# Optimization experiments

Measured on AMD Instinct MI355X. Metric: run time of the kernel, lower is better.

The kernel has to match this reference:

```python
import jax, jax.numpy as jnp
import numpy as np

B, OBS, H, A, E = 131072, 194, 64, 5, 3  # batch, obs dim, hidden, max_action_dim, n event types


def setup_inputs() -> dict:
    key = jax.random.key(0)
    ks = jax.random.split(key, 16)
    s = lambda k, shape, std=0.1: (jax.random.normal(k, shape, dtype=jnp.float32) * std)
    return {
        "x": jax.random.normal(ks[0], (B, OBS), dtype=jnp.float32),
        "action": jax.random.randint(ks[1], (B,), 0, A),
        "W1": s(ks[2], (OBS, H)), "b1": jnp.zeros((H,), jnp.float32),
        "W2": s(ks[3], (H, H)),   "b2": jnp.zeros((H,), jnp.float32),
        "Wh": s(ks[4], (E, H, A), 0.01), "bh": jnp.zeros((E, A), jnp.float32),
        "Wc1": s(ks[5], (OBS, H)), "bc1": jnp.zeros((H,), jnp.float32),
        "Wc2": s(ks[6], (H, H)),   "bc2": jnp.zeros((H,), jnp.float32),
        "Wc3": s(ks[7], (H, 1)),   "bc3": jnp.zeros((1,), jnp.float32),
    }


def reference(x, action, W1, b1, W2, b2, Wh, bh, Wc1, bc1, Wc2, bc2, Wc3, bc3):
    # shared trunk
    feat = jnp.tanh(jnp.tanh(x @ W1 + b1) @ W2 + b2)          # [B, H]
    # route each sample to one of E heads via argmax of first 3 obs dims
    ev = jnp.argmax(x[:, :E], axis=1)                          # [B] int
    all_logits = jnp.einsum('bh,eha->bea', feat, Wh) + bh      # [B, E, A]
    logits = jnp.take_along_axis(
        all_logits, jnp.broadcast_to(ev[:, None, None], (x.shape[0], 1, A)), axis=1
    )[:, 0]                                                    # [B, A]
    logp_all = jax.nn.log_softmax(logits, axis=-1)             # [B, A]
    logp = jnp.take_along_axis(logp_all, action[:, None], axis=1)[:, 0]  # [B]
    entropy = -jnp.sum(jnp.exp(logp_all) * logp_all, axis=-1)  # [B]
    # critic
    value = jnp.tanh(jnp.tanh(x @ Wc1 + bc1) @ Wc2 + bc2) @ Wc3 + bc3    # [B, 1]
    return action, logp, entropy, value
```

## Files before the change

### kernel.cpp

```cpp
#include <hip/hip_runtime.h>
#include <hip/hip_bf16.h>

constexpr int Bt  = 131072;
constexpr int OBS = 194;
constexpr int Hd  = 64;
constexpr int NT  = 256;
constexpr int MT  = 64;
constexpr int HS  = 72;
constexpr int LS  = 18;

constexpr int W1B_OFF  = 0;
constexpr int WC1B_OFF = 28672;
constexpr int W2B_OFF  = 57344;
constexpr int WC2B_OFF = 65536;
constexpr int WHB_OFF  = 73728;

typedef short bf8   __attribute__((ext_vector_type(8)));
typedef float f32x4 __attribute__((ext_vector_type(4)));

__device__ __forceinline__ short f2bs(float f) {
    union { __hip_bfloat16 h; short s; } u;
    u.h = __float2bfloat16(f);
    return u.s;
}
__device__ __forceinline__ float bs2f(short s) {
    union { short s; __hip_bfloat16 h; } u;
    u.s = s;
    return __bfloat162float(u.h);
}
__device__ __forceinline__ float fast_tanh(float v) {
    v = fminf(fmaxf(v, -15.f), 15.f);
    float e = __expf(2.f * v);
    return (e - 1.f) * __builtin_amdgcn_rcpf(e + 1.f);
}

__global__ void __launch_bounds__(256) prep(
    const float* __restrict__ W1, const float* __restrict__ W2,
    const float* __restrict__ Wh, const float* __restrict__ Wc1,
    const float* __restrict__ Wc2, const float* __restrict__ Wc3,
    short* __restrict__ ws)
{
    const int gid = blockIdx.x * 256 + threadIdx.x;
    const int gsz = gridDim.x * 256;

    for (int i = gid; i < 28672; i += gsz) {
        int j = i & 7, l = (i >> 3) & 63, nt = (i >> 9) & 3, kb = i >> 11;
        int k = kb * 32 + ((l >> 4) << 3) + j;
        int n = nt * 16 + (l & 15);
        short v1 = 0, v2 = 0;
        if (k < OBS) {
            v1 = f2bs(W1[k * 64 + n]);
            v2 = f2bs(Wc1[k * 64 + n]);
        }
        ws[W1B_OFF + i]  = v1;
        ws[WC1B_OFF + i] = v2;
    }
    for (int i = gid; i < 8192; i += gsz) {
        int j = i & 7, l = (i >> 3) & 63, nt = (i >> 9) & 3, kb = i >> 11;
        int k = kb * 32 + ((l >> 4) << 3) + j;
        int n = nt * 16 + (l & 15);
        ws[W2B_OFF + i]  = f2bs(W2[k * 64 + n]);
        ws[WC2B_OFF + i] = f2bs(Wc2[k * 64 + n]);
    }
    for (int i = gid; i < 1024; i += gsz) {
        int j = i & 7, l = (i >> 3) & 63, kb = i >> 9;
        int k = kb * 32 + ((l >> 4) << 3) + j;
        int cc = l & 15;
        float v;
        if (cc == 15) v = Wc3[k];
        else { int e = cc / 5, a = cc - 5 * e; v = Wh[(e * 64 + k) * 5 + a]; }
        ws[WHB_OFF + i] = f2bs(v);
    }
}

__global__ void __launch_bounds__(NT, 4) fused_ac(
    const float* __restrict__ x, const int* __restrict__ act_in,
    const float* __restrict__ b1, const float* __restrict__ b2,
    const float* __restrict__ bh, const float* __restrict__ bc1,
    const float* __restrict__ bc2, const float* __restrict__ bc3,
    const short* __restrict__ ws,
    float* __restrict__ out)
{
    __shared__ __align__(16) short hA[4][16 * HS];
    __shared__ __align__(16) short hC[4][16 * HS];
    __shared__ short logitb[4][16 * LS];
    __shared__ float valb[4][16];

    const int t  = threadIdx.x;
    const int w  = t >> 6;
    const int l  = t & 63;
    const int q  = l >> 4;
    const int c  = l & 15;
    const int b0 = blockIdx.x * MT;

    const bf8* __restrict__ fW1  = reinterpret_cast<const bf8*>(ws + W1B_OFF);
    const bf8* __restrict__ fWc1 = reinterpret_cast<const bf8*>(ws + WC1B_OFF);
    const bf8* __restrict__ fW2  = reinterpret_cast<const bf8*>(ws + W2B_OFF);
    const bf8* __restrict__ fWc2 = reinterpret_cast<const bf8*>(ws + WC2B_OFF);
    const bf8* __restrict__ fWh  = reinterpret_cast<const bf8*>(ws + WHB_OFF);

    short* ha = hA[w];
    short* hc = hC[w];

    f32x4 aa[4], ac[4];
    #pragma unroll
    for (int nt = 0; nt < 4; ++nt) {
        aa[nt] = f32x4{0.f, 0.f, 0.f, 0.f};
        ac[nt] = f32x4{0.f, 0.f, 0.f, 0.f};
    }
    {
        const float* xr = x + (size_t)(b0 + w * 16 + c) * OBS;
        #pragma unroll
        for (int kb = 0; kb < 6; ++kb) {
            const float2* p = reinterpret_cast<const float2*>(xr + kb * 32 + q * 8);
            float2 v0 = p[0], v1 = p[1], v2 = p[2], v3 = p[3];
            bf8 a;
            a[0] = f2bs(v0.x); a[1] = f2bs(v0.y); a[2] = f2bs(v1.x); a[3] = f2bs(v1.y);
            a[4] = f2bs(v2.x); a[5] = f2bs(v2.y); a[6] = f2bs(v3.x); a[7] = f2bs(v3.y);
            #pragma unroll
            for (int nt = 0; nt < 4; ++nt) {
                aa[nt] = __builtin_amdgcn_mfma_f32_16x16x32_bf16(a, fW1 [(kb * 4 + nt) * 64 + l], aa[nt], 0, 0, 0);
                ac[nt] = __builtin_amdgcn_mfma_f32_16x16x32_bf16(a, fWc1[(kb * 4 + nt) * 64 + l], ac[nt], 0, 0, 0);
            }
        }
        bf8 a6 = {0, 0, 0, 0, 0, 0, 0, 0};
        if (q == 0) {
            float2 v = *reinterpret_cast<const float2*>(xr + 192);
            a6[0] = f2bs(v.x); a6[1] = f2bs(v.y);
        }
        #pragma unroll
        for (int nt = 0; nt < 4; ++nt) {
            aa[nt] = __builtin_amdgcn_mfma_f32_16x16x32_bf16(a6, fW1 [(6 * 4 + nt) * 64 + l], aa[nt], 0, 0, 0);
            ac[nt] = __builtin_amdgcn_mfma_f32_16x16x32_bf16(a6, fWc1[(6 * 4 + nt) * 64 + l], ac[nt], 0, 0, 0);
        }
    }
    #pragma unroll
    for (int nt = 0; nt < 4; ++nt) {
        float ba = b1[nt * 16 + c], bc = bc1[nt * 16 + c];
        #pragma unroll
        for (int r = 0; r < 4; ++r) {
            ha[(q * 4 + r) * HS + nt * 16 + c] = f2bs(fast_tanh(aa[nt][r] + ba));
            hc[(q * 4 + r) * HS + nt * 16 + c] = f2bs(fast_tanh(ac[nt][r] + bc));
        }
    }

    #pragma unroll
    for (int nt = 0; nt < 4; ++nt) {
        aa[nt] = f32x4{0.f, 0.f, 0.f, 0.f};
        ac[nt] = f32x4{0.f, 0.f, 0.f, 0.f};
    }
    #pragma unroll
    for (int kb = 0; kb < 2; ++kb) {
        bf8 xa = *reinterpret_cast<const bf8*>(&ha[c * HS + kb * 32 + q * 8]);
        bf8 xc = *reinterpret_cast<const bf8*>(&hc[c * HS + kb * 32 + q * 8]);
        #pragma unroll
        for (int nt = 0; nt < 4; ++nt) {
            aa[nt] = __builtin_amdgcn_mfma_f32_16x16x32_bf16(xa, fW2 [(kb * 4 + nt) * 64 + l], aa[nt], 0, 0, 0);
            ac[nt] = __builtin_amdgcn_mfma_f32_16x16x32_bf16(xc, fWc2[(kb * 4 + nt) * 64 + l], ac[nt], 0, 0, 0);
        }
    }
    #pragma unroll
    for (int nt = 0; nt < 4; ++nt) {
        float ba = b2[nt * 16 + c], bc = bc2[nt * 16 + c];
        #pragma unroll
        for (int r = 0; r < 4; ++r) {
            ha[(q * 4 + r) * HS + nt * 16 + c] = f2bs(fast_tanh(aa[nt][r] + ba));
            hc[(q * 4 + r) * HS + nt * 16 + c] = f2bs(fast_tanh(ac[nt][r] + bc));
        }
    }

    {
        f32x4 lg = f32x4{0.f, 0.f, 0.f, 0.f};
        f32x4 vv = f32x4{0.f, 0.f, 0.f, 0.f};
        #pragma unroll
        for (int kb = 0; kb < 2; ++kb) {
            bf8 bw = fWh[kb * 64 + l];
            bf8 fa = *reinterpret_cast<const bf8*>(&ha[c * HS + kb * 32 + q * 8]);
            bf8 fc = *reinterpret_cast<const bf8*>(&hc[c * HS + kb * 32 + q * 8]);
            lg = __builtin_amdgcn_mfma_f32_16x16x32_bf16(fa, bw, lg, 0, 0, 0);
            vv = __builtin_amdgcn_mfma_f32_16x16x32_bf16(fc, bw, vv, 0, 0, 0);
        }
        short* lw = logitb[w];
        #pragma unroll
        for (int r = 0; r < 4; ++r)
            lw[(q * 4 + r) * LS + c] = f2bs(lg[r]);
        if (c == 15) {
            float bc3v = bc3[0];
            #pragma unroll
            for (int r = 0; r < 4; ++r)
                valb[w][q * 4 + r] = vv[r] + bc3v;
        }
    }

    {
        int m  = c;
        int gm = b0 + w * 16 + m;
        const float* xr = x + (size_t)gm * OBS;
        float x0 = xr[0], x1 = xr[1], x2 = xr[2];
        int ev = 0; float best = x0;
        if (x1 > best) { best = x1; ev = 1; }
        if (x2 > best) { ev = 2; }
        const short* lw = logitb[w];
        float lg[5];
        #pragma unroll
        for (int a = 0; a < 5; ++a)
            lg[a] = bs2f(lw[m * LS + ev * 5 + a]) + bh[ev * 5 + a];
        float mx = lg[0];
        #pragma unroll
        for (int a = 1; a < 5; ++a) mx = fmaxf(mx, lg[a]);
        float se = 0.f;
        #pragma unroll
        for (int a = 0; a < 5; ++a) se += __expf(lg[a] - mx);
        float lse = __logf(se) + mx;
        int act = act_in[gm];
        float lsel = lg[0];
        #pragma unroll
        for (int a = 1; a < 5; ++a) lsel = (act == a) ? lg[a] : lsel;
        float ent = 0.f;
        #pragma unroll
        for (int a = 0; a < 5; ++a) { float lp = lg[a] - lse; ent -= __expf(lp) * lp; }

        if (l < 16) {
            out[gm]          = (float)act;
            out[Bt + gm]     = lsel - lse;
            out[2 * Bt + gm] = ent;
            out[3 * Bt + gm] = valb[w][m];
        }
    }
}

extern "C" void kernel_launch(void* const* d_in, const int* in_sizes, int n_in,
                              void* d_out, int out_size, void* d_ws, size_t ws_size,
                              hipStream_t stream) {
    const float* x   = (const float*)d_in[0];
    const int*   act = (const int*)  d_in[1];
    const float* W1  = (const float*)d_in[2];
    const float* b1  = (const float*)d_in[3];
    const float* W2  = (const float*)d_in[4];
    const float* b2  = (const float*)d_in[5];
    const float* Wh  = (const float*)d_in[6];
    const float* bh  = (const float*)d_in[7];
    const float* Wc1 = (const float*)d_in[8];
    const float* bc1 = (const float*)d_in[9];
    const float* Wc2 = (const float*)d_in[10];
    const float* bc2 = (const float*)d_in[11];
    const float* Wc3 = (const float*)d_in[12];
    const float* bc3 = (const float*)d_in[13];
    float* out = (float*)d_out;
    short* ws  = (short*)d_ws;

    hipLaunchKernelGGL(prep, dim3(64), dim3(256), 0, stream,
                       W1, W2, Wh, Wc1, Wc2, Wc3, ws);
    hipLaunchKernelGGL(fused_ac, dim3(Bt / MT), dim3(NT), 0, stream,
                       x, act, b1, b2, bh, bc1, bc2, bc3, ws, out);
}
```

Before: 201.9 us.

## Fold biases into MFMA, permute hidden layout for packed stores, shrink blocks

Folds the layer-1 bias into the padded K slot of the weight matrix, with a constant 1 appended to the input. Initializes the layer-2 and head accumulators with their biases. Permutes the hidden-unit order in the W2 and head weight packing so each lane can write four consecutive bf16 activations with one packed 64-bit LDS store, using paired bf16 conversion. Computes the argmax event from the x values already loaded, dropping the second global read of x, and reduces blocks to 128 threads with a higher occupancy hint. These changes cut scalar LDS stores, conversions, bias adds and redundant global loads, but rounding the bias to bf16 adds small precision error.

```diff
diff --git a/kernel.cpp b/kernel.cpp
--- a/kernel.cpp
+++ b/kernel.cpp
@@ -3,10 +3,9 @@
 
 constexpr int Bt  = 131072;
 constexpr int OBS = 194;
-constexpr int Hd  = 64;
-constexpr int NT  = 256;
-constexpr int MT  = 64;
-constexpr int HS  = 72;
+constexpr int NT  = 128;
+constexpr int MT  = 32;
+constexpr int RS  = 72;
 constexpr int LS  = 18;
 
 constexpr int W1B_OFF  = 0;
@@ -17,6 +16,7 @@
 
 typedef short bf8   __attribute__((ext_vector_type(8)));
 typedef float f32x4 __attribute__((ext_vector_type(4)));
+typedef unsigned int u32;
 
 __device__ __forceinline__ short f2bs(float f) {
     union { __hip_bfloat16 h; short s; } u;
@@ -28,6 +28,11 @@
     u.s = s;
     return __bfloat162float(u.h);
 }
+__device__ __forceinline__ u32 pk2(float a, float b) {
+    union { __hip_bfloat162 h; u32 u; } r;
+    r.h = __float22bfloat162_rn(float2{a, b});
+    return r.u;
+}
 __device__ __forceinline__ float fast_tanh(float v) {
     v = fminf(fmaxf(v, -15.f), 15.f);
     float e = __expf(2.f * v);
@@ -35,8 +40,9 @@
 }
 
 __global__ void __launch_bounds__(256) prep(
-    const float* __restrict__ W1, const float* __restrict__ W2,
-    const float* __restrict__ Wh, const float* __restrict__ Wc1,
+    const float* __restrict__ W1, const float* __restrict__ b1,
+    const float* __restrict__ W2, const float* __restrict__ Wh,
+    const float* __restrict__ Wc1, const float* __restrict__ bc1,
     const float* __restrict__ Wc2, const float* __restrict__ Wc3,
     short* __restrict__ ws)
 {
@@ -51,47 +57,51 @@
         if (k < OBS) {
             v1 = f2bs(W1[k * 64 + n]);
             v2 = f2bs(Wc1[k * 64 + n]);
+        } else if (k == OBS) {
+            v1 = f2bs(b1[n]);
+            v2 = f2bs(bc1[n]);
         }
         ws[W1B_OFF + i]  = v1;
         ws[WC1B_OFF + i] = v2;
     }
     for (int i = gid; i < 8192; i += gsz) {
         int j = i & 7, l = (i >> 3) & 63, nt = (i >> 9) & 3, kb = i >> 11;
-        int k = kb * 32 + ((l >> 4) << 3) + j;
+        int s = kb * 32 + ((l >> 4) << 3) + j;
+        int kp = (s & 3) * 16 + (s >> 2);
         int n = nt * 16 + (l & 15);
-        ws[W2B_OFF + i]  = f2bs(W2[k * 64 + n]);
-        ws[WC2B_OFF + i] = f2bs(Wc2[k * 64 + n]);
+        ws[W2B_OFF + i]  = f2bs(W2[kp * 64 + n]);
+        ws[WC2B_OFF + i] = f2bs(Wc2[kp * 64 + n]);
     }
     for (int i = gid; i < 1024; i += gsz) {
         int j = i & 7, l = (i >> 3) & 63, kb = i >> 9;
-        int k = kb * 32 + ((l >> 4) << 3) + j;
+        int s = kb * 32 + ((l >> 4) << 3) + j;
+        int kp = (s & 3) * 16 + (s >> 2);
         int cc = l & 15;
         float v;
-        if (cc == 15) v = Wc3[k];
-        else { int e = cc / 5, a = cc - 5 * e; v = Wh[(e * 64 + k) * 5 + a]; }
+        if (cc == 15) v = Wc3[kp];
+        else { int e = cc / 5, a = cc - 5 * e; v = Wh[(e * 64 + kp) * 5 + a]; }
         ws[WHB_OFF + i] = f2bs(v);
     }
 }
 
-__global__ void __launch_bounds__(NT, 4) fused_ac(
+__global__ void __launch_bounds__(NT, 7) fused_ac(
     const float* __restrict__ x, const int* __restrict__ act_in,
-    const float* __restrict__ b1, const float* __restrict__ b2,
-    const float* __restrict__ bh, const float* __restrict__ bc1,
-    const float* __restrict__ bc2, const float* __restrict__ bc3,
+    const float* __restrict__ b2, const float* __restrict__ bc2,
+    const float* __restrict__ bh, const float* __restrict__ bc3,
     const short* __restrict__ ws,
     float* __restrict__ out)
 {
-    __shared__ __align__(16) short hA[4][16 * HS];
-    __shared__ __align__(16) short hC[4][16 * HS];
-    __shared__ short logitb[4][16 * LS];
-    __shared__ float valb[4][16];
+    __shared__ __align__(16) short hA[2][16 * RS];
+    __shared__ __align__(16) short hC[2][16 * RS];
+    __shared__ short logitb[2][16 * LS];
+    __shared__ float valb[2][16];
 
     const int t  = threadIdx.x;
     const int w  = t >> 6;
     const int l  = t & 63;
     const int q  = l >> 4;
     const int c  = l & 15;
-    const int b0 = blockIdx.x * MT;
+    const int gm = blockIdx.x * MT + w * 16 + c;
 
     const bf8* __restrict__ fW1  = reinterpret_cast<const bf8*>(ws + W1B_OFF);
     const bf8* __restrict__ fWc1 = reinterpret_cast<const bf8*>(ws + WC1B_OFF);
@@ -99,8 +109,15 @@
     const bf8* __restrict__ fWc2 = reinterpret_cast<const bf8*>(ws + WC2B_OFF);
     const bf8* __restrict__ fWh  = reinterpret_cast<const bf8*>(ws + WHB_OFF);
 
-    short* ha = hA[w];
-    short* hc = hC[w];
+    float b2v[4], bc2v[4];
+    #pragma unroll
+    for (int nt = 0; nt < 4; ++nt) {
+        b2v[nt]  = b2[nt * 16 + c];
+        bc2v[nt] = bc2[nt * 16 + c];
+    }
+    float bhv = (c < 15) ? bh[c] : bc3[0];
+    int act = 0;
+    if (l < 16) act = act_in[gm];
 
     f32x4 aa[4], ac[4];
     #pragma unroll
@@ -108,51 +125,64 @@
         aa[nt] = f32x4{0.f, 0.f, 0.f, 0.f};
         ac[nt] = f32x4{0.f, 0.f, 0.f, 0.f};
     }
+    int ev = 0;
     {
-        const float* xr = x + (size_t)(b0 + w * 16 + c) * OBS;
+        const float* xr = x + (size_t)gm * OBS;
         #pragma unroll
         for (int kb = 0; kb < 6; ++kb) {
             const float2* p = reinterpret_cast<const float2*>(xr + kb * 32 + q * 8);
             float2 v0 = p[0], v1 = p[1], v2 = p[2], v3 = p[3];
-            bf8 a;
-            a[0] = f2bs(v0.x); a[1] = f2bs(v0.y); a[2] = f2bs(v1.x); a[3] = f2bs(v1.y);
-            a[4] = f2bs(v2.x); a[5] = f2bs(v2.y); a[6] = f2bs(v3.x); a[7] = f2bs(v3.y);
+            if (kb == 0 && q == 0) {
+                float best = v0.x;
+                if (v0.y > best) { best = v0.y; ev = 1; }
+                if (v1.x > best) { ev = 2; }
+            }
+            union { bf8 v; u32 u[4]; } a;
+            a.u[0] = pk2(v0.x, v0.y); a.u[1] = pk2(v1.x, v1.y);
+            a.u[2] = pk2(v2.x, v2.y); a.u[3] = pk2(v3.x, v3.y);
             #pragma unroll
             for (int nt = 0; nt < 4; ++nt) {
-                aa[nt] = __builtin_amdgcn_mfma_f32_16x16x32_bf16(a, fW1 [(kb * 4 + nt) * 64 + l], aa[nt], 0, 0, 0);
-                ac[nt] = __builtin_amdgcn_mfma_f32_16x16x32_bf16(a, fWc1[(kb * 4 + nt) * 64 + l], ac[nt], 0, 0, 0);
+                aa[nt] = __builtin_amdgcn_mfma_f32_16x16x32_bf16(a.v, fW1 [(kb * 4 + nt) * 64 + l], aa[nt], 0, 0, 0);
+                ac[nt] = __builtin_amdgcn_mfma_f32_16x16x32_bf16(a.v, fWc1[(kb * 4 + nt) * 64 + l], ac[nt], 0, 0, 0);
             }
         }
-        bf8 a6 = {0, 0, 0, 0, 0, 0, 0, 0};
+        union { bf8 v; u32 u[4]; } a;
+        a.u[0] = 0; a.u[1] = 0; a.u[2] = 0; a.u[3] = 0;
         if (q == 0) {
             float2 v = *reinterpret_cast<const float2*>(xr + 192);
-            a6[0] = f2bs(v.x); a6[1] = f2bs(v.y);
+            a.u[0] = pk2(v.x, v.y);
+            a.u[1] = pk2(1.0f, 0.0f);
         }
         #pragma unroll
         for (int nt = 0; nt < 4; ++nt) {
-            aa[nt] = __builtin_amdgcn_mfma_f32_16x16x32_bf16(a6, fW1 [(6 * 4 + nt) * 64 + l], aa[nt], 0, 0, 0);
-            ac[nt] = __builtin_amdgcn_mfma_f32_16x16x32_bf16(a6, fWc1[(6 * 4 + nt) * 64 + l], ac[nt], 0, 0, 0);
-        }
-    }
+            aa[nt] = __builtin_amdgcn_mfma_f32_16x16x32_bf16(a.v, fW1 [(6 * 4 + nt) * 64 + l], aa[nt], 0, 0, 0);
+            ac[nt] = __builtin_amdgcn_mfma_f32_16x16x32_bf16(a.v, fWc1[(6 * 4 + nt) * 64 + l], ac[nt], 0, 0, 0);
+        }
+    }
+
+    short* ha = hA[w];
+    short* hc = hC[w];
+
+    #pragma unroll
+    for (int r = 0; r < 4; ++r) {
+        uint2 pa, pc;
+        pa.x = pk2(fast_tanh(aa[0][r]), fast_tanh(aa[1][r]));
+        pa.y = pk2(fast_tanh(aa[2][r]), fast_tanh(aa[3][r]));
+        pc.x = pk2(fast_tanh(ac[0][r]), fast_tanh(ac[1][r]));
+        pc.y = pk2(fast_tanh(ac[2][r]), fast_tanh(ac[3][r]));
+        *reinterpret_cast<uint2*>(&ha[(q * 4 + r) * RS + 4 * c]) = pa;
+        *reinterpret_cast<uint2*>(&hc[(q * 4 + r) * RS + 4 * c]) = pc;
+    }
+
     #pragma unroll
     for (int nt = 0; nt < 4; ++nt) {
-        float ba = b1[nt * 16 + c], bc = bc1[nt * 16 + c];
-        #pragma unroll
-        for (int r = 0; r < 4; ++r) {
-            ha[(q * 4 + r) * HS + nt * 16 + c] = f2bs(fast_tanh(aa[nt][r] + ba));
-            hc[(q * 4 + r) * HS + nt * 16 + c] = f2bs(fast_tanh(ac[nt][r] + bc));
-        }
-    }
-
-    #pragma unroll
-    for (int nt = 0; nt < 4; ++nt) {
-        aa[nt] = f32x4{0.f, 0.f, 0.f, 0.f};
-        ac[nt] = f32x4{0.f, 0.f, 0.f, 0.f};
+        aa[nt] = f32x4{b2v[nt], b2v[nt], b2v[nt], b2v[nt]};
+        ac[nt] = f32x4{bc2v[nt], bc2v[nt], bc2v[nt], bc2v[nt]};
     }
     #pragma unroll
     for (int kb = 0; kb < 2; ++kb) {
-        bf8 xa = *reinterpret_cast<const bf8*>(&ha[c * HS + kb * 32 + q * 8]);
-        bf8 xc = *reinterpret_cast<const bf8*>(&hc[c * HS + kb * 32 + q * 8]);
+        bf8 xa = *reinterpret_cast<const bf8*>(&ha[c * RS + kb * 32 + q * 8]);
+        bf8 xc = *reinterpret_cast<const bf8*>(&hc[c * RS + kb * 32 + q * 8]);
         #pragma unroll
         for (int nt = 0; nt < 4; ++nt) {
             aa[nt] = __builtin_amdgcn_mfma_f32_16x16x32_bf16(xa, fW2 [(kb * 4 + nt) * 64 + l], aa[nt], 0, 0, 0);
@@ -160,23 +190,24 @@
         }
     }
     #pragma unroll
-    for (int nt = 0; nt < 4; ++nt) {
-        float ba = b2[nt * 16 + c], bc = bc2[nt * 16 + c];
-        #pragma unroll
-        for (int r = 0; r < 4; ++r) {
-            ha[(q * 4 + r) * HS + nt * 16 + c] = f2bs(fast_tanh(aa[nt][r] + ba));
-            hc[(q * 4 + r) * HS + nt * 16 + c] = f2bs(fast_tanh(ac[nt][r] + bc));
-        }
+    for (int r = 0; r < 4; ++r) {
+        uint2 pa, pc;
+        pa.x = pk2(fast_tanh(aa[0][r]), fast_tanh(aa[1][r]));
+        pa.y = pk2(fast_tanh(aa[2][r]), fast_tanh(aa[3][r]));
+        pc.x = pk2(fast_tanh(ac[0][r]), fast_tanh(ac[1][r]));
+        pc.y = pk2(fast_tanh(ac[2][r]), fast_tanh(ac[3][r]));
+        *reinterpret_cast<uint2*>(&ha[(q * 4 + r) * RS + 4 * c]) = pa;
+        *reinterpret_cast<uint2*>(&hc[(q * 4 + r) * RS + 4 * c]) = pc;
     }
 
     {
-        f32x4 lg = f32x4{0.f, 0.f, 0.f, 0.f};
-        f32x4 vv = f32x4{0.f, 0.f, 0.f, 0.f};
+        f32x4 lg = f32x4{bhv, bhv, bhv, bhv};
+        f32x4 vv = f32x4{bhv, bhv, bhv, bhv};
         #pragma unroll
         for (int kb = 0; kb < 2; ++kb) {
             bf8 bw = fWh[kb * 64 + l];
-            bf8 fa = *reinterpret_cast<const bf8*>(&ha[c * HS + kb * 32 + q * 8]);
-            bf8 fc = *reinterpret_cast<const bf8*>(&hc[c * HS + kb * 32 + q * 8]);
+            bf8 fa = *reinterpret_cast<const bf8*>(&ha[c * RS + kb * 32 + q * 8]);
+            bf8 fc = *reinterpret_cast<const bf8*>(&hc[c * RS + kb * 32 + q * 8]);
             lg = __builtin_amdgcn_mfma_f32_16x16x32_bf16(fa, bw, lg, 0, 0, 0);
             vv = __builtin_amdgcn_mfma_f32_16x16x32_bf16(fc, bw, vv, 0, 0, 0);
         }
@@ -185,26 +216,18 @@
         for (int r = 0; r < 4; ++r)
             lw[(q * 4 + r) * LS + c] = f2bs(lg[r]);
         if (c == 15) {
-            float bc3v = bc3[0];
             #pragma unroll
             for (int r = 0; r < 4; ++r)
-                valb[w][q * 4 + r] = vv[r] + bc3v;
-        }
-    }
-
-    {
-        int m  = c;
-        int gm = b0 + w * 16 + m;
-        const float* xr = x + (size_t)gm * OBS;
-        float x0 = xr[0], x1 = xr[1], x2 = xr[2];
-        int ev = 0; float best = x0;
-        if (x1 > best) { best = x1; ev = 1; }
-        if (x2 > best) { ev = 2; }
+                valb[w][q * 4 + r] = vv[r];
+        }
+    }
+
+    if (l < 16) {
         const short* lw = logitb[w];
         float lg[5];
         #pragma unroll
         for (int a = 0; a < 5; ++a)
-            lg[a] = bs2f(lw[m * LS + ev * 5 + a]) + bh[ev * 5 + a];
+            lg[a] = bs2f(lw[c * LS + ev * 5 + a]);
         float mx = lg[0];
         #pragma unroll
         for (int a = 1; a < 5; ++a) mx = fmaxf(mx, lg[a]);
@@ -212,7 +235,6 @@
         #pragma unroll
         for (int a = 0; a < 5; ++a) se += __expf(lg[a] - mx);
         float lse = __logf(se) + mx;
-        int act = act_in[gm];
         float lsel = lg[0];
         #pragma unroll
         for (int a = 1; a < 5; ++a) lsel = (act == a) ? lg[a] : lsel;
@@ -220,12 +242,10 @@
         #pragma unroll
         for (int a = 0; a < 5; ++a) { float lp = lg[a] - lse; ent -= __expf(lp) * lp; }
 
-        if (l < 16) {
-            out[gm]          = (float)act;
-            out[Bt + gm]     = lsel - lse;
-            out[2 * Bt + gm] = ent;
-            out[3 * Bt + gm] = valb[w][m];
-        }
+        out[gm]          = (float)act;
+        out[Bt + gm]     = lsel - lse;
+        out[2 * Bt + gm] = ent;
+        out[3 * Bt + gm] = valb[w][c];
     }
 }
 
@@ -250,7 +270,7 @@
     short* ws  = (short*)d_ws;
 
     hipLaunchKernelGGL(prep, dim3(64), dim3(256), 0, stream,
-                       W1, W2, Wh, Wc1, Wc2, Wc3, ws);
+                       W1, b1, W2, Wh, Wc1, bc1, Wc2, Wc3, ws);
     hipLaunchKernelGGL(fused_ac, dim3(Bt / MT), dim3(NT), 0, stream,
-                       x, act, b1, b2, bh, bc1, bc2, bc3, ws, out);
-}
+                       x, act, b2, bc2, bh, bc3, ws, out);
+}
```

After: 233.7 us. 1.16x slower.
